# Kernel optimization log

Hardware: AMD Instinct MI355X
Metric: run time of the kernel (lower is better)

The kernel has to match this reference:

```python
import jax, jax.numpy as jnp
import numpy as np


def _resize_bilinear_align_corners(x, out_size):
    # x: [B, C, h, w] -> [B, C, out_size, out_size], matches F.interpolate(mode='bilinear', align_corners=True)
    def axis_interp(arr, size_in, size_out, axis):
        coords = jnp.linspace(0.0, size_in - 1.0, size_out)
        i0 = jnp.floor(coords).astype(jnp.int32)
        i1 = jnp.minimum(i0 + 1, size_in - 1)
        t = (coords - i0).astype(arr.dtype)
        a0 = jnp.take(arr, i0, axis=axis)
        a1 = jnp.take(arr, i1, axis=axis)
        shape = [1] * arr.ndim
        shape[axis] = size_out
        t = t.reshape(shape)
        return a0 * (1.0 - t) + a1 * t

    B, C, h, w = x.shape
    x = axis_interp(x, h, out_size, 2)
    x = axis_interp(x, w, out_size, 3)
    return x


def _similarity_matrix(x, sp, num):
    # Torch: mean_values[i][j] = mean(x[i][sp_repeated[i] == j], dim=0)
    # Boolean indexing flattens across channels, so this is a SCALAR mean over
    # (channels x segment pixels), broadcast to all C channels.
    B, C, H, W = x.shape
    xs = x.sum(axis=1).reshape(B, H * W)          # sum over channels, per pixel
    ids = sp.reshape(B, H * W)
    seg_sum = jax.vmap(
        lambda v, i: jax.ops.segment_sum(v, i, num_segments=num))(xs, ids)
    cnt = jax.vmap(
        lambda i: jax.ops.segment_sum(jnp.ones(i.shape, x.dtype), i,
                                      num_segments=num))(ids)
    m = seg_sum / (cnt * C)                        # [B, num] scalar mean per segment
    # diff vector over channels has identical entries -> norm(diff)/sqrt(C) == |m_i - m_j|
    return 1.0 - jnp.abs(m[:, :, None] - m[:, None, :])  # [B, num, num]


def reference(input, feature, sp, num):
    feature = _resize_bilinear_align_corners(feature, input.shape[-1])
    mat1 = _similarity_matrix(input, sp, num)
    mat2 = _similarity_matrix(feature, sp, num)
    return jnp.mean(jnp.abs(mat1 - mat2))


def setup_inputs() -> dict:
    key = jax.random.key(0)
    k1, k2, k3 = jax.random.split(key, 3)
    B, C_in, H, W = 8, 64, 256, 256
    C_feat, hf, wf = 256, 64, 64
    num = 256
    return {
        "input": jax.random.normal(k1, (B, C_in, H, W), dtype=jnp.float32),
        "feature": jax.random.normal(k2, (B, C_feat, hf, wf), dtype=jnp.float32),
        "sp": jax.random.randint(k3, (B, 1, H, W), 0, num, dtype=jnp.int32),
        "num": num,
    }
```

## Files before the change

kernel.cpp:

```cpp
#include <hip/hip_runtime.h>

#define NB 8
#define C_IN 64
#define HW 65536
#define CF 256
#define FHW 4096
#define NSEG 256
#define MBLK 64
#define MAGIC 0x13579BDFu
#define AG __HIP_MEMORY_SCOPE_AGENT


__global__ __launch_bounds__(256) void featsum_kernel(
    const float* __restrict__ feat, float* __restrict__ fsum) {
  __shared__ float4 lred[256];
  int b = blockIdx.y, e = blockIdx.x, t = threadIdx.x;
  int q = t & 63, cg = t >> 6;
  const float4* f4 = (const float4*)(feat + (size_t)b * CF * FHW);
  int col = e * 64 + q;
  float4 s = make_float4(0.f, 0.f, 0.f, 0.f);
#pragma unroll 8
  for (int c = cg; c < CF; c += 4) {
    float4 v = f4[(size_t)c * (FHW / 4) + col];
    s.x += v.x; s.y += v.y; s.z += v.z; s.w += v.w;
  }
  lred[cg * 64 + q] = s;
  __syncthreads();
  if (t < 64) {
    float4 a = lred[t], b1 = lred[64 + t], c1 = lred[128 + t], d = lred[192 + t];
    a.x += b1.x + c1.x + d.x; a.y += b1.y + c1.y + d.y;
    a.z += b1.z + c1.z + d.z; a.w += b1.w + c1.w + d.w;
    ((float4*)fsum)[(size_t)b * (FHW / 4) + e * 64 + t] = a;
  }
}

__global__ __launch_bounds__(256) void main_kernel(
    const float* __restrict__ input, const int* __restrict__ sp,
    const float* __restrict__ fsum, float* __restrict__ seg_part) {
  __shared__ float fls[FHW];
  __shared__ float bin[3][NSEG];
  int b = blockIdx.y, blk = blockIdx.x, t = threadIdx.x;
  {
    const float4* s4 = (const float4*)(fsum + (size_t)b * FHW);
    float4* d4 = (float4*)fls;
#pragma unroll
    for (int i = 0; i < 4; ++i) d4[i * 256 + t] = s4[i * 256 + t];
  }
  bin[0][t] = 0.f; bin[1][t] = 0.f; bin[2][t] = 0.f;
  __syncthreads();

  int v0 = blk * 256 + t;
  const float4* in4 = (const float4*)(input + (size_t)b * C_IN * HW);
  float4 xs = make_float4(0.f, 0.f, 0.f, 0.f);
#pragma unroll
  for (int c = 0; c < C_IN; ++c) {
    float4 v = in4[(size_t)c * (HW / 4) + v0];
    xs.x += v.x; xs.y += v.y; xs.z += v.z; xs.w += v.w;
  }
  int4 sv = ((const int4*)(sp + (size_t)b * HW))[v0];
  atomicAdd(&bin[0][sv.x], xs.x); atomicAdd(&bin[1][sv.x], 1.f);
  atomicAdd(&bin[0][sv.y], xs.y); atomicAdd(&bin[1][sv.y], 1.f);
  atomicAdd(&bin[0][sv.z], xs.z); atomicAdd(&bin[1][sv.z], 1.f);
  atomicAdd(&bin[0][sv.w], xs.w); atomicAdd(&bin[1][sv.w], 1.f);

  int p0 = v0 * 4;
  int y = p0 >> 8;
  float cy = (float)y * (63.0f / 255.0f);
  int iy = (int)cy; float ty = cy - (float)iy; int iy1 = min(iy + 1, 63);
  int svv[4] = {sv.x, sv.y, sv.z, sv.w};
#pragma unroll
  for (int kk = 0; kk < 4; ++kk) {
    int x = (p0 + kk) & 255;
    float cx = (float)x * (63.0f / 255.0f);
    int ix = (int)cx; float tx = cx - (float)ix; int ix1 = min(ix + 1, 63);
    float f00 = fls[iy * 64 + ix],  f10 = fls[iy1 * 64 + ix];
    float f01 = fls[iy * 64 + ix1], f11 = fls[iy1 * 64 + ix1];
    float a0 = f00 * (1.f - ty) + f10 * ty;
    float a1 = f01 * (1.f - ty) + f11 * ty;
    atomicAdd(&bin[2][svv[kk]], a0 * (1.f - tx) + a1 * tx);
  }
  __syncthreads();
  float* sb = seg_part + (size_t)(b * MBLK + blk) * 3 * NSEG;
  sb[t]            = bin[0][t];
  sb[NSEG + t]     = bin[1][t];
  sb[2 * NSEG + t] = bin[2][t];
}

__global__ __launch_bounds__(1024) void pairfinal_kernel(
    const float* __restrict__ seg_part,
    unsigned* __restrict__ ppbits, unsigned* __restrict__ bflags,
    float* __restrict__ out) {
  __shared__ float s3[3 * NSEG];
  __shared__ float m1[NSEG], m2[NSEG];
  __shared__ float red[16];
  int b = blockIdx.x, t = threadIdx.x;
  if (t < 3 * NSEG) {
    const float* base = seg_part + (size_t)b * MBLK * 3 * NSEG + t;
    float s = 0.f;
#pragma unroll
    for (int k = 0; k < MBLK; ++k) s += base[k * 3 * NSEG];
    s3[t] = s;
  }
  __syncthreads();
  if (t < NSEG) {
    float cnt = s3[NSEG + t];
    m1[t] = s3[t] / (cnt * 64.0f);
    m2[t] = s3[2 * NSEG + t] / (cnt * 256.0f);
  }
  __syncthreads();
  int i = t & 255, j0 = (t >> 8) * 64;
  float a1 = m1[i], a2 = m2[i], acc = 0.f;
#pragma unroll
  for (int jj = 0; jj < 64; ++jj) {
    int j = j0 + jj;
    acc += fabsf(fabsf(a1 - m1[j]) - fabsf(a2 - m2[j]));
  }
#pragma unroll
  for (int off = 32; off; off >>= 1) acc += __shfl_down(acc, off);
  if ((t & 63) == 0) red[t >> 6] = acc;
  __syncthreads();
  if (t == 0) {
    float s = 0.f;
#pragma unroll
    for (int w = 0; w < 16; ++w) s += red[w];
    __hip_atomic_store(&ppbits[b], __float_as_uint(s), __ATOMIC_RELAXED, AG);
    __hip_atomic_store(&bflags[b], MAGIC, __ATOMIC_RELEASE, AG);
    if (b == 0) {
      float tot = s;
      for (int ob = 1; ob < NB; ++ob) {
        while (__hip_atomic_load(&bflags[ob], __ATOMIC_ACQUIRE, AG) != MAGIC)
          __builtin_amdgcn_s_sleep(2);
        tot += __uint_as_float(__hip_atomic_load(
            &ppbits[ob], __ATOMIC_RELAXED, AG));
        __hip_atomic_store(&bflags[ob], 0u, __ATOMIC_RELAXED, AG);
      }
      out[0] = tot / 524288.0f;
      __hip_atomic_store(&bflags[0], 0u, __ATOMIC_RELAXED, AG);
    }
  }
}

extern "C" void kernel_launch(void* const* d_in, const int* in_sizes, int n_in,
                              void* d_out, int out_size, void* d_ws, size_t ws_size,
                              hipStream_t stream) {
  const float* input   = (const float*)d_in[0];
  const float* feature = (const float*)d_in[1];
  const int*   sp      = (const int*)d_in[2];
  float* ws = (float*)d_ws;
  float*    fsum     = ws;
  float*    seg_part = ws + (size_t)NB * FHW;
  unsigned* ppbits   = (unsigned*)(seg_part + (size_t)NB * MBLK * 3 * NSEG);
  unsigned* bflags   = ppbits + NB;

  featsum_kernel<<<dim3(16, NB), 256, 0, stream>>>(feature, fsum);
  main_kernel<<<dim3(MBLK, NB), 256, 0, stream>>>(input, sp, fsum, seg_part);
  pairfinal_kernel<<<dim3(NB), 1024, 0, stream>>>(seg_part, ppbits, bflags,
                                                  (float*)d_out);
}
```

Before: 50.54 us.

## Split channel reduction across more blocks and accumulate segments with global atomics

The input channel sum is split into 4 channel groups per pixel tile, and the feature upsampling runs in separate blocks, giving 320 blocks per batch instead of 64. featsum now uses 64 blocks per batch and also zeroes the global segment accumulators. Per-block partial arrays are replaced by global atomicAdd into per-batch segment sums, so the final kernel no longer loops over 64 partials and can run with 256 threads. The aim is more memory-level parallelism to hide latency. The cost is global atomic contention and floating-point results that depend on atomic ordering.

```diff
diff --git a/kernel.cpp b/kernel.cpp
--- a/kernel.cpp
+++ b/kernel.cpp
@@ -6,63 +6,97 @@
 #define CF 256
 #define FHW 4096
 #define NSEG 256
-#define MBLK 64
+#define CPG 16
+#define CGRP 4
+#define PBLK 64
 #define MAGIC 0x13579BDFu
 #define AG __HIP_MEMORY_SCOPE_AGENT
 
 
 __global__ __launch_bounds__(256) void featsum_kernel(
-    const float* __restrict__ feat, float* __restrict__ fsum) {
+    const float* __restrict__ feat, float* __restrict__ fsum,
+    float* __restrict__ sxg, float* __restrict__ scg,
+    float* __restrict__ sfg) {
   __shared__ float4 lred[256];
+  __shared__ float4 lred2[64];
   int b = blockIdx.y, e = blockIdx.x, t = threadIdx.x;
-  int q = t & 63, cg = t >> 6;
+  if (e < 3) {
+    float* z = (e == 0) ? sxg : (e == 1) ? scg : sfg;
+    z[b * NSEG + t] = 0.f;
+  }
+  int q = t & 15, cg = t >> 4;
   const float4* f4 = (const float4*)(feat + (size_t)b * CF * FHW);
-  int col = e * 64 + q;
+  int col = e * 16 + q;
   float4 s = make_float4(0.f, 0.f, 0.f, 0.f);
-#pragma unroll 8
-  for (int c = cg; c < CF; c += 4) {
-    float4 v = f4[(size_t)c * (FHW / 4) + col];
+#pragma unroll
+  for (int k = 0; k < 16; ++k) {
+    float4 v = f4[(size_t)(cg + k * 16) * (FHW / 4) + col];
     s.x += v.x; s.y += v.y; s.z += v.z; s.w += v.w;
   }
-  lred[cg * 64 + q] = s;
+  lred[cg * 16 + q] = s;
   __syncthreads();
   if (t < 64) {
-    float4 a = lred[t], b1 = lred[64 + t], c1 = lred[128 + t], d = lred[192 + t];
+    int q2 = t & 15, g2 = t >> 4;
+    float4 a = lred[(g2 * 4 + 0) * 16 + q2];
+    float4 b1 = lred[(g2 * 4 + 1) * 16 + q2];
+    float4 c1 = lred[(g2 * 4 + 2) * 16 + q2];
+    float4 d = lred[(g2 * 4 + 3) * 16 + q2];
     a.x += b1.x + c1.x + d.x; a.y += b1.y + c1.y + d.y;
     a.z += b1.z + c1.z + d.z; a.w += b1.w + c1.w + d.w;
-    ((float4*)fsum)[(size_t)b * (FHW / 4) + e * 64 + t] = a;
+    lred2[t] = a;
+  }
+  __syncthreads();
+  if (t < 16) {
+    float4 a = lred2[t], b1 = lred2[16 + t], c1 = lred2[32 + t], d = lred2[48 + t];
+    a.x += b1.x + c1.x + d.x; a.y += b1.y + c1.y + d.y;
+    a.z += b1.z + c1.z + d.z; a.w += b1.w + c1.w + d.w;
+    ((float4*)fsum)[(size_t)b * (FHW / 4) + col] = a;
   }
 }
 
 __global__ __launch_bounds__(256) void main_kernel(
     const float* __restrict__ input, const int* __restrict__ sp,
-    const float* __restrict__ fsum, float* __restrict__ seg_part) {
+    const float* __restrict__ fsum, float* __restrict__ sxg,
+    float* __restrict__ scg, float* __restrict__ sfg) {
   __shared__ float fls[FHW];
-  __shared__ float bin[3][NSEG];
-  int b = blockIdx.y, blk = blockIdx.x, t = threadIdx.x;
+  __shared__ float bx[NSEG];
+  __shared__ float bc[NSEG], bf[NSEG];
+  int b = blockIdx.y, x = blockIdx.x, t = threadIdx.x;
+  const int4* sp4 = (const int4*)(sp + (size_t)b * HW);
+
+  if (x < PBLK * CGRP) {
+    int pix = x >> 2, g = x & 3;
+    bx[t] = 0.f;
+    __syncthreads();
+    int v0 = pix * 256 + t;
+    const float4* in4 = (const float4*)(input + (size_t)b * C_IN * HW);
+    float4 xs = make_float4(0.f, 0.f, 0.f, 0.f);
+#pragma unroll
+    for (int k = 0; k < CPG; ++k) {
+      float4 v = in4[(size_t)(g * CPG + k) * (HW / 4) + v0];
+      xs.x += v.x; xs.y += v.y; xs.z += v.z; xs.w += v.w;
+    }
+    int4 sv = sp4[v0];
+    atomicAdd(&bx[sv.x], xs.x);
+    atomicAdd(&bx[sv.y], xs.y);
+    atomicAdd(&bx[sv.z], xs.z);
+    atomicAdd(&bx[sv.w], xs.w);
+    __syncthreads();
+    atomicAdd(&sxg[b * NSEG + t], bx[t]);
+    return;
+  }
+
+  int pix = x - PBLK * CGRP;
   {
     const float4* s4 = (const float4*)(fsum + (size_t)b * FHW);
     float4* d4 = (float4*)fls;
 #pragma unroll
     for (int i = 0; i < 4; ++i) d4[i * 256 + t] = s4[i * 256 + t];
   }
-  bin[0][t] = 0.f; bin[1][t] = 0.f; bin[2][t] = 0.f;
+  bc[t] = 0.f; bf[t] = 0.f;
   __syncthreads();
-
-  int v0 = blk * 256 + t;
-  const float4* in4 = (const float4*)(input + (size_t)b * C_IN * HW);
-  float4 xs = make_float4(0.f, 0.f, 0.f, 0.f);
-#pragma unroll
-  for (int c = 0; c < C_IN; ++c) {
-    float4 v = in4[(size_t)c * (HW / 4) + v0];
-    xs.x += v.x; xs.y += v.y; xs.z += v.z; xs.w += v.w;
-  }
-  int4 sv = ((const int4*)(sp + (size_t)b * HW))[v0];
-  atomicAdd(&bin[0][sv.x], xs.x); atomicAdd(&bin[1][sv.x], 1.f);
-  atomicAdd(&bin[0][sv.y], xs.y); atomicAdd(&bin[1][sv.y], 1.f);
-  atomicAdd(&bin[0][sv.z], xs.z); atomicAdd(&bin[1][sv.z], 1.f);
-  atomicAdd(&bin[0][sv.w], xs.w); atomicAdd(&bin[1][sv.w], 1.f);
-
+  int v0 = pix * 256 + t;
+  int4 sv = sp4[v0];
   int p0 = v0 * 4;
   int y = p0 >> 8;
   float cy = (float)y * (63.0f / 255.0f);
@@ -70,59 +104,45 @@
   int svv[4] = {sv.x, sv.y, sv.z, sv.w};
 #pragma unroll
   for (int kk = 0; kk < 4; ++kk) {
-    int x = (p0 + kk) & 255;
-    float cx = (float)x * (63.0f / 255.0f);
+    int xx = (p0 + kk) & 255;
+    float cx = (float)xx * (63.0f / 255.0f);
     int ix = (int)cx; float tx = cx - (float)ix; int ix1 = min(ix + 1, 63);
     float f00 = fls[iy * 64 + ix],  f10 = fls[iy1 * 64 + ix];
     float f01 = fls[iy * 64 + ix1], f11 = fls[iy1 * 64 + ix1];
     float a0 = f00 * (1.f - ty) + f10 * ty;
     float a1 = f01 * (1.f - ty) + f11 * ty;
-    atomicAdd(&bin[2][svv[kk]], a0 * (1.f - tx) + a1 * tx);
+    atomicAdd(&bf[svv[kk]], a0 * (1.f - tx) + a1 * tx);
+    atomicAdd(&bc[svv[kk]], 1.f);
   }
   __syncthreads();
-  float* sb = seg_part + (size_t)(b * MBLK + blk) * 3 * NSEG;
-  sb[t]            = bin[0][t];
-  sb[NSEG + t]     = bin[1][t];
-  sb[2 * NSEG + t] = bin[2][t];
+  atomicAdd(&scg[b * NSEG + t], bc[t]);
+  atomicAdd(&sfg[b * NSEG + t], bf[t]);
 }
 
-__global__ __launch_bounds__(1024) void pairfinal_kernel(
-    const float* __restrict__ seg_part,
+__global__ __launch_bounds__(256) void pairfinal_kernel(
+    const float* __restrict__ sxg, const float* __restrict__ scg,
+    const float* __restrict__ sfg,
     unsigned* __restrict__ ppbits, unsigned* __restrict__ bflags,
     float* __restrict__ out) {
-  __shared__ float s3[3 * NSEG];
   __shared__ float m1[NSEG], m2[NSEG];
-  __shared__ float red[16];
+  __shared__ float red[4];
   int b = blockIdx.x, t = threadIdx.x;
-  if (t < 3 * NSEG) {
-    const float* base = seg_part + (size_t)b * MBLK * 3 * NSEG + t;
-    float s = 0.f;
-#pragma unroll
-    for (int k = 0; k < MBLK; ++k) s += base[k * 3 * NSEG];
-    s3[t] = s;
+  {
+    float cnt = scg[b * NSEG + t];
+    m1[t] = sxg[b * NSEG + t] / (cnt * 64.0f);
+    m2[t] = sfg[b * NSEG + t] / (cnt * 256.0f);
   }
   __syncthreads();
-  if (t < NSEG) {
-    float cnt = s3[NSEG + t];
-    m1[t] = s3[t] / (cnt * 64.0f);
-    m2[t] = s3[2 * NSEG + t] / (cnt * 256.0f);
-  }
-  __syncthreads();
-  int i = t & 255, j0 = (t >> 8) * 64;
-  float a1 = m1[i], a2 = m2[i], acc = 0.f;
-#pragma unroll
-  for (int jj = 0; jj < 64; ++jj) {
-    int j = j0 + jj;
+  float a1 = m1[t], a2 = m2[t], acc = 0.f;
+#pragma unroll 8
+  for (int j = 0; j < NSEG; ++j)
     acc += fabsf(fabsf(a1 - m1[j]) - fabsf(a2 - m2[j]));
-  }
 #pragma unroll
   for (int off = 32; off; off >>= 1) acc += __shfl_down(acc, off);
   if ((t & 63) == 0) red[t >> 6] = acc;
   __syncthreads();
   if (t == 0) {
-    float s = 0.f;
-#pragma unroll
-    for (int w = 0; w < 16; ++w) s += red[w];
+    float s = red[0] + red[1] + red[2] + red[3];
     __hip_atomic_store(&ppbits[b], __float_as_uint(s), __ATOMIC_RELAXED, AG);
     __hip_atomic_store(&bflags[b], MAGIC, __ATOMIC_RELEASE, AG);
     if (b == 0) {
@@ -147,13 +167,16 @@
   const float* feature = (const float*)d_in[1];
   const int*   sp      = (const int*)d_in[2];
   float* ws = (float*)d_ws;
-  float*    fsum     = ws;
-  float*    seg_part = ws + (size_t)NB * FHW;
-  unsigned* ppbits   = (unsigned*)(seg_part + (size_t)NB * MBLK * 3 * NSEG);
-  unsigned* bflags   = ppbits + NB;
+  float*    fsum   = ws;
+  float*    sxg    = ws + 32768;
+  float*    scg    = ws + 34816;
+  float*    sfg    = ws + 36864;
+  unsigned* ppbits = (unsigned*)(ws + 38912);
+  unsigned* bflags = ppbits + NB;
 
-  featsum_kernel<<<dim3(16, NB), 256, 0, stream>>>(feature, fsum);
-  main_kernel<<<dim3(MBLK, NB), 256, 0, stream>>>(input, sp, fsum, seg_part);
-  pairfinal_kernel<<<dim3(NB), 1024, 0, stream>>>(seg_part, ppbits, bflags,
-                                                  (float*)d_out);
+  featsum_kernel<<<dim3(64, NB), 256, 0, stream>>>(feature, fsum, sxg, scg, sfg);
+  main_kernel<<<dim3(PBLK * CGRP + PBLK, NB), 256, 0, stream>>>(
+      input, sp, fsum, sxg, scg, sfg);
+  pairfinal_kernel<<<dim3(NB), 256, 0, stream>>>(sxg, scg, sfg, ppbits, bflags,
+                                                 (float*)d_out);
 }
```

Measured after the change: 53.85 us. +6.5%, slower.
